# Performance work log

Measured on AMD Instinct MI355X. Metric: run time of the kernel, lower is better.

## Reference

```python
import jax, jax.numpy as jnp
import numpy as np

B, T, K, H = 8192, 96, 32, 768  # batch, max_len, output_dim (tags), bert hidden


def setup_inputs() -> dict:
    key = jax.random.key(0)
    k1, k2, k3, k4 = jax.random.split(key, 4)
    hidden = jax.random.normal(k1, (B, H), dtype=jnp.float32)
    target = jax.random.randint(k2, (B, T), 0, K, dtype=jnp.int32)
    # Dense(output_dim * max_len) params
    W = jax.random.normal(k3, (H, T * K), dtype=jnp.float32) * 0.02
    b = jnp.zeros((T * K,), dtype=jnp.float32)
    # tf.random.uniform transition matrix
    transitions = jax.random.uniform(k4, (K, K), dtype=jnp.float32)
    return {"hidden": hidden, "target": target, "W": W, "b": b, "transitions": transitions}


def _crf_log_norm(em_tm, transitions):
    # em_tm: [T, B, K] time-major emissions. Forward algorithm (logsumexp recurrence).
    def step(alpha, em_t):
        # alpha: [B, K]; broadcast over next-tag axis
        new = jax.nn.logsumexp(alpha[:, :, None] + transitions[None, :, :], axis=1) + em_t
        return new, None
    alpha, _ = jax.lax.scan(step, em_tm[0], em_tm[1:])
    return jax.nn.logsumexp(alpha, axis=-1)  # [B]


def _crf_sequence_score(em_btk, target, transitions):
    # unary: emission score at gold tags; binary: transition scores along gold path
    unary = jnp.take_along_axis(em_btk, target[..., None], axis=-1)[..., 0].sum(-1)
    binary = transitions[target[:, :-1], target[:, 1:]].sum(-1)
    return unary + binary  # [B]


def _viterbi_decode(em_tm, transitions):
    # em_tm: [T, B, K]. Max-product forward pass collecting backpointers.
    def fwd(v, em_t):
        scores = v[:, :, None] + transitions[None, :, :]  # [B, K_prev, K_next]
        bp = jnp.argmax(scores, axis=1).astype(jnp.int32)  # [B, K]
        return jnp.max(scores, axis=1) + em_t, bp
    v, bps = jax.lax.scan(fwd, em_tm[0], em_tm[1:])  # bps: [T-1, B, K]
    last_tag = jnp.argmax(v, axis=-1).astype(jnp.int32)  # [B]
    # backtrace (reverse scan); output index i is the tag at time i
    def back(tag, bp_t):
        prev = jnp.take_along_axis(bp_t, tag[:, None], axis=1)[:, 0]
        return prev, prev
    _, prevs = jax.lax.scan(back, last_tag, bps, reverse=True)  # [T-1, B]
    tags = jnp.concatenate([prevs, last_tag[None, :]], axis=0)  # [T, B]
    return jnp.transpose(tags), jnp.max(v, axis=-1)


def reference(hidden, target, W, b, transitions):
    # Dense with sigmoid, then reshape to (B, max_len, output_dim)
    em = jax.nn.sigmoid(hidden @ W + b).reshape(hidden.shape[0], T, K)
    em_tm = jnp.transpose(em, (1, 0, 2))  # time-major for scan
    log_likelihood = _crf_sequence_score(em, target, transitions) - _crf_log_norm(em_tm, transitions)
    decode_predict, _ = _viterbi_decode(em_tm, transitions)
    return decode_predict, log_likelihood
```

## Files before the change

### kernel.cpp

```cpp
#include <hip/hip_runtime.h>
#include <cstdint>
#include <cstddef>

#define B_  8192
#define T_  96
#define K_  32
#define H_  768
#define NK_ (T_ * K_)

typedef __attribute__((ext_vector_type(8))) _Float16 f16x8;
typedef __attribute__((ext_vector_type(4))) float    f32x4;

#define SCALE_UP   4096.0f
#define SCALE_DOWN (1.0f / 16777216.0f)

__device__ __forceinline__ void load_lds16(const void* g, void* l) {
    __builtin_amdgcn_global_load_lds(
        (const __attribute__((address_space(1))) unsigned int*)g,
        (__attribute__((address_space(3))) unsigned int*)l,
        16, 0, 0);
}

__global__ __launch_bounds__(256) void splitA_kernel(
    const float* __restrict__ A, _Float16* __restrict__ Ath, _Float16* __restrict__ Atl)
{
    const int g   = blockIdx.x * 256 + threadIdx.x;
    const int row = g / 96;
    const int o   = g - row * 96;
    const int ks  = o >> 2, qq = o & 3;
    const int r   = row & 127, rb = row >> 7;
    const size_t dst = (size_t)(rb * 24 + ks) * 4096 + r * 32 + ((qq ^ ((r >> 1) & 3)) << 3);

    f32x4 v0 = *(const f32x4*)(A + (size_t)row * H_ + o * 8);
    f32x4 v1 = *(const f32x4*)(A + (size_t)row * H_ + o * 8 + 4);
    f16x8 hi, lo;
#pragma unroll
    for (int e = 0; e < 8; e++) {
        float x = ((e < 4) ? v0[e] : v1[e - 4]) * SCALE_UP;
        _Float16 h = (_Float16)x;
        hi[e] = h;
        lo[e] = (_Float16)(x - (float)h);
    }
    *(f16x8*)&Ath[dst] = hi;
    *(f16x8*)&Atl[dst] = lo;
}

__global__ __launch_bounds__(256) void splitW_kernel(
    const float* __restrict__ W, _Float16* __restrict__ Wth, _Float16* __restrict__ Wtl)
{
    const int g   = blockIdx.x * 256 + threadIdx.x;
    const int ko  = g / NK_;
    const int col = g - ko * NK_;
    const int k0  = ko * 8;
    const int cb  = col >> 7, n = col & 127;
    const int ks  = k0 >> 5, qq = (k0 & 31) >> 3;
    const size_t dst = (size_t)(cb * 24 + ks) * 4096 + n * 32 + ((qq ^ ((n >> 1) & 3)) << 3);

    f16x8 hi, lo;
#pragma unroll
    for (int j = 0; j < 8; j++) {
        float x = W[(size_t)(k0 + j) * NK_ + col] * SCALE_UP;
        _Float16 h = (_Float16)x;
        hi[j] = h;
        lo[j] = (_Float16)(x - (float)h);
    }
    *(f16x8*)&Wth[dst] = hi;
    *(f16x8*)&Wtl[dst] = lo;
}

__global__ __launch_bounds__(256, 2) void gemm_mfma_sigmoid_kernel(
    const _Float16* __restrict__ Ath, const _Float16* __restrict__ Atl,
    const _Float16* __restrict__ Wth, const _Float16* __restrict__ Wtl,
    const float* __restrict__ bias, float* __restrict__ em)
{
    __shared__ _Float16 lds[2][4][4096];

    const int tid  = threadIdx.x;
    const int cb   = blockIdx.x;
    const int rb   = blockIdx.y;
    const int lane = tid & 63;
    const int w    = tid >> 6;
    const int wr   = w >> 1, wc = w & 1;
    const int fr   = lane & 15;
    const int kg   = lane >> 4;

    const _Float16* srcs[4] = {
        Ath + (size_t)(rb * 24) * 4096, Atl + (size_t)(rb * 24) * 4096,
        Wth + (size_t)(cb * 24) * 4096, Wtl + (size_t)(cb * 24) * 4096 };

    auto stage = [&](int ks, int bb) {
#pragma unroll
        for (int m = 0; m < 4; m++) {
            const _Float16* s = srcs[m] + (size_t)ks * 4096 + w * 1024 + lane * 8;
            _Float16* d = &lds[bb][m][w * 1024];
            load_lds16(s, d);
            load_lds16(s + 512, d + 512);
        }
    };

    f32x4 acc[4][4];
#pragma unroll
    for (int i = 0; i < 4; i++)
#pragma unroll
        for (int j = 0; j < 4; j++) acc[i][j] = (f32x4)0.0f;

    int cur = 0;
    stage(0, 0);

    for (int ks = 0; ks < 24; ks++) {
        __syncthreads();
        if (ks + 1 < 24) stage(ks + 1, cur ^ 1);

        f16x8 fah[4], fal[4], fbh[4], fbl[4];
#pragma unroll
        for (int mi = 0; mi < 4; mi++) {
            const int r   = wr * 64 + mi * 16 + fr;
            const int idx = r * 32 + ((kg ^ ((r >> 1) & 3)) << 3);
            fah[mi] = *(const f16x8*)&lds[cur][0][idx];
            fal[mi] = *(const f16x8*)&lds[cur][1][idx];
        }
#pragma unroll
        for (int ni = 0; ni < 4; ni++) {
            const int r   = wc * 64 + ni * 16 + fr;
            const int idx = r * 32 + ((kg ^ ((r >> 1) & 3)) << 3);
            fbh[ni] = *(const f16x8*)&lds[cur][2][idx];
            fbl[ni] = *(const f16x8*)&lds[cur][3][idx];
        }
#pragma unroll
        for (int mi = 0; mi < 4; mi++)
#pragma unroll
            for (int ni = 0; ni < 4; ni++) {
                acc[mi][ni] = __builtin_amdgcn_mfma_f32_16x16x32_f16(fah[mi], fbh[ni], acc[mi][ni], 0, 0, 0);
                acc[mi][ni] = __builtin_amdgcn_mfma_f32_16x16x32_f16(fah[mi], fbl[ni], acc[mi][ni], 0, 0, 0);
                acc[mi][ni] = __builtin_amdgcn_mfma_f32_16x16x32_f16(fal[mi], fbh[ni], acc[mi][ni], 0, 0, 0);
            }
        cur ^= 1;
    }

    const int er = rb * 128 + wr * 64 + (lane >> 4) * 4;
    const int ec = cb * 128 + wc * 64 + fr;
#pragma unroll
    for (int ni = 0; ni < 4; ni++) {
        const int   gc = ec + ni * 16;
        const float bv = bias[gc];
#pragma unroll
        for (int mi = 0; mi < 4; mi++)
#pragma unroll
            for (int r = 0; r < 4; r++) {
                const int gr = er + mi * 16 + r;
                float x = acc[mi][ni][r] * SCALE_DOWN + bv;
                em[(size_t)gr * NK_ + gc] = 1.0f / (1.0f + __expf(-x));
            }
    }
}

__global__ __launch_bounds__(256) void crf_scan_kernel(
    const float* __restrict__ em,
    const int* __restrict__ target,
    const float* __restrict__ trans,
    float* __restrict__ out_tags,
    float* __restrict__ ll)
{
    __shared__ float  trans_s[K_ * K_];
    __shared__ float4 ev4[8][16];
    __shared__ unsigned int bp_s[8][24][K_];

    const int tid = threadIdx.x;
    const int g   = tid >> 5;
    const int k   = tid & 31;
    const int b   = blockIdx.x * 8 + g;

    for (int i = tid; i < K_ * K_; i += 256) trans_s[i] = trans[i];
    __syncthreads();

    float tcol[K_], Ecol[K_];
#pragma unroll
    for (int p = 0; p < K_; p++) {
        tcol[p] = trans_s[p * K_ + k];
        Ecol[p] = __expf(tcol[p]);
    }

    const float* emb = em + (size_t)b * NK_;

    const float em0 = emb[k];
    float alpha = em0;
    float v     = em0;
    int   tgt_prev = target[b * T_];
    float unary  = (k == tgt_prev) ? em0 : 0.0f;
    float binary = 0.0f;
    unsigned int bpw = 0;

    float2* evp = (float2*)&ev4[g][0];

    for (int t = 1; t < T_; t++) {
        const float em_t = emb[t * K_ + k];

        float mh = alpha;
#pragma unroll
        for (int d = 16; d >= 1; d >>= 1) mh = fmaxf(mh, __shfl_xor(mh, d));
        const float e = __expf(alpha - mh);

        evp[k] = make_float2(e, v);
        __builtin_amdgcn_wave_barrier();

        float sum = 0.0f;
        float bv  = -1e30f;
        int   bi  = 0;
#pragma unroll
        for (int c = 0; c < 16; c++) {
            f32x4 q = *(const f32x4*)&ev4[g][c];
            const int p0 = 2 * c, p1 = 2 * c + 1;
            sum = fmaf(q[0], Ecol[p0], sum);
            float sv0 = q[1] + tcol[p0];
            if (sv0 > bv) { bv = sv0; bi = p0; }
            sum = fmaf(q[2], Ecol[p1], sum);
            float sv1 = q[3] + tcol[p1];
            if (sv1 > bv) { bv = sv1; bi = p1; }
        }

        alpha = mh + __logf(sum) + em_t;
        v     = bv + em_t;

        bpw |= (unsigned int)bi << (8 * ((t - 1) & 3));
        if (((t - 1) & 3) == 3) { bp_s[g][(t - 1) >> 2][k] = bpw; bpw = 0; }

        const int tgt = target[b * T_ + t];
        unary  += (k == tgt) ? em_t : 0.0f;
        binary += trans_s[tgt_prev * K_ + tgt];
        tgt_prev = tgt;
    }
    bp_s[g][23][k] = bpw;
    __builtin_amdgcn_wave_barrier();

    float m2 = alpha;
#pragma unroll
    for (int d = 16; d >= 1; d >>= 1) m2 = fmaxf(m2, __shfl_xor(m2, d));
    float s2 = __expf(alpha - m2);
#pragma unroll
    for (int d = 16; d >= 1; d >>= 1) s2 += __shfl_xor(s2, d);
    const float logZ = m2 + __logf(s2);

    float un = unary;
#pragma unroll
    for (int d = 16; d >= 1; d >>= 1) un += __shfl_xor(un, d);

    float bvv = v;
    int   bii = k;
#pragma unroll
    for (int d = 16; d >= 1; d >>= 1) {
        float ov = __shfl_xor(bvv, d);
        int   oi = __shfl_xor(bii, d);
        if (ov > bvv || (ov == bvv && oi < bii)) { bvv = ov; bii = oi; }
    }

    if (k == 0) {
        ll[b] = un + binary - logZ;
        float* ot = out_tags + (size_t)b * T_;
        int tag = bii;
        ot[T_ - 1] = (float)tag;
        for (int t = T_ - 2; t >= 0; t--) {
            unsigned int wd = bp_s[g][t >> 2][tag];
            tag = (wd >> (8 * (t & 3))) & 0xFF;
            ot[t] = (float)tag;
        }
    }
}

extern "C" void kernel_launch(void* const* d_in, const int* in_sizes, int n_in,
                              void* d_out, int out_size, void* d_ws, size_t ws_size,
                              hipStream_t stream)
{
    const float* hidden = (const float*)d_in[0];
    const int*   target = (const int*)d_in[1];
    const float* W      = (const float*)d_in[2];
    const float* bias   = (const float*)d_in[3];
    const float* trans  = (const float*)d_in[4];

    float* out      = (float*)d_out;
    float* out_tags = out;
    float* out_ll   = out + (size_t)B_ * T_;

    char* ws = (char*)d_ws;
    const size_t emB = (size_t)B_ * NK_ * 4;
    const size_t ahB = (size_t)B_ * H_ * 2;
    const size_t whB = (size_t)H_ * NK_ * 2;
    float*    em  = (float*)ws;
    _Float16* Ath = (_Float16*)(ws + emB);
    _Float16* Atl = (_Float16*)(ws + emB + ahB);
    _Float16* Wth = (_Float16*)(ws + emB + 2 * ahB);
    _Float16* Wtl = (_Float16*)(ws + emB + 2 * ahB + whB);

    splitA_kernel<<<(B_ * 96) / 256, 256, 0, stream>>>(hidden, Ath, Atl);
    splitW_kernel<<<(NK_ * 96) / 256, 256, 0, stream>>>(W, Wth, Wtl);

    dim3 gemm_grid(NK_ / 128, B_ / 128);
    gemm_mfma_sigmoid_kernel<<<gemm_grid, 256, 0, stream>>>(Ath, Atl, Wth, Wtl, bias, em);

    crf_scan_kernel<<<B_ / 8, 256, 0, stream>>>(em, target, trans, out_tags, out_ll);
}
```

Baseline: 300.8 us.

## Split CRF scan into forward and Viterbi waves, remap GEMM tiles per XCD

The CRF kernel now gives the forward (log-normalizer) recurrence and the Viterbi recurrence to separate wavefronts, so each sequence's two chains run in parallel rather than serially in one thread group. The forward pass moves to the linear exp domain with periodic power-of-two renormalization, which removes the per-step max, exp and log. The gold-path score is computed in parallel across time, and backpointers are packed at 5 bits each. The GEMM grid is flattened with a block-index swizzle that spreads neighbouring tiles across XCDs. This adds numerical risk from the exp-domain recurrence with its fixed offset of 4 per step.

New measurement: 250.5 us. -16.7%, faster.

```diff
diff --git a/kernel.cpp b/kernel.cpp
--- a/kernel.cpp
+++ b/kernel.cpp
@@ -76,8 +76,10 @@
     __shared__ _Float16 lds[2][4][4096];
 
     const int tid  = threadIdx.x;
-    const int cb   = blockIdx.x;
-    const int rb   = blockIdx.y;
+    const int bid  = blockIdx.x;
+    const int wgid = (bid & 7) * 192 + (bid >> 3);
+    const int cb   = wgid % 24;
+    const int rb   = wgid / 24;
     const int lane = tid & 63;
     const int w    = tid >> 6;
     const int wr   = w >> 1, wc = w & 1;
@@ -154,114 +156,165 @@
     }
 }
 
-__global__ __launch_bounds__(256) void crf_scan_kernel(
+
+#define VSTEP(T_, SH_, WI_)                                               \
+  {                                                                       \
+    const float cem = na; na = emb[((T_) + 1) * K_];                      \
+    vxs[k] = va;                                                          \
+    __builtin_amdgcn_wave_barrier();                                      \
+    float bva = -1e30f; int bia = 0;                                      \
+    _Pragma("unroll")                                                     \
+    for (int j = 0; j < 8; j++) {                                         \
+      f32x4 vq = *(const f32x4*)&vxs[4 * j];                              \
+      float s0 = vq[0] + tca[4 * j];                                      \
+      float s1 = vq[1] + tca[4 * j + 1];                                  \
+      float s2 = vq[2] + tca[4 * j + 2];                                  \
+      float s3 = vq[3] + tca[4 * j + 3];                                  \
+      float w0 = (s1 > s0) ? s1 : s0;                                     \
+      int   i0 = (s1 > s0) ? (4 * j + 1) : (4 * j);                       \
+      float w1 = (s3 > s2) ? s3 : s2;                                     \
+      int   i1 = (s3 > s2) ? (4 * j + 3) : (4 * j + 2);                   \
+      if (w1 > w0) { w0 = w1; i0 = i1; }                                  \
+      if (w0 > bva) { bva = w0; bia = i0; }                               \
+    }                                                                     \
+    va = bva + cem;                                                       \
+    bpw |= (unsigned int)bia << (5 * (SH_));                              \
+    if ((SH_) == 5) { bps[k * 17 + (WI_)] = bpw; bpw = 0; }               \
+    __builtin_amdgcn_wave_barrier();                                      \
+  }
+
+__global__ __launch_bounds__(256, 4) void crf_roles_kernel(
     const float* __restrict__ em,
     const int* __restrict__ target,
     const float* __restrict__ trans,
     float* __restrict__ out_tags,
     float* __restrict__ ll)
 {
-    __shared__ float  trans_s[K_ * K_];
-    __shared__ float4 ev4[8][16];
-    __shared__ unsigned int bp_s[8][24][K_];
-
-    const int tid = threadIdx.x;
-    const int g   = tid >> 5;
-    const int k   = tid & 31;
-    const int b   = blockIdx.x * 8 + g;
+    __shared__ float trans_s[K_ * K_];
+    __shared__ float Eex[4][36];
+    __shared__ float vex[4][36];
+    __shared__ unsigned int bp5[4][545];
+    __shared__ unsigned char tgt_s[4][T_];
+
+    const int tid  = threadIdx.x;
+    const int w    = tid >> 6;
+    const int lane = tid & 63;
+    const int half = lane >> 5;
+    const int k    = lane & 31;
+    const bool isFwd = (w < 2);
+    const int s    = (((isFwd ? w : w - 2) << 1) | half);
+    const int b    = blockIdx.x * 4 + s;
 
     for (int i = tid; i < K_ * K_; i += 256) trans_s[i] = trans[i];
     __syncthreads();
 
-    float tcol[K_], Ecol[K_];
-#pragma unroll
-    for (int p = 0; p < K_; p++) {
-        tcol[p] = trans_s[p * K_ + k];
-        Ecol[p] = __expf(tcol[p]);
-    }
-
-    const float* emb = em + (size_t)b * NK_;
-
-    const float em0 = emb[k];
-    float alpha = em0;
-    float v     = em0;
-    int   tgt_prev = target[b * T_];
-    float unary  = (k == tgt_prev) ? em0 : 0.0f;
-    float binary = 0.0f;
-    unsigned int bpw = 0;
-
-    float2* evp = (float2*)&ev4[g][0];
-
-    for (int t = 1; t < T_; t++) {
-        const float em_t = emb[t * K_ + k];
-
-        float mh = alpha;
-#pragma unroll
-        for (int d = 16; d >= 1; d >>= 1) mh = fmaxf(mh, __shfl_xor(mh, d));
-        const float e = __expf(alpha - mh);
-
-        evp[k] = make_float2(e, v);
+    const float* emb = em + (size_t)b * NK_ + k;
+
+    if (isFwd) {
+        float Ea2[K_];
+#pragma unroll
+        for (int p = 0; p < K_; p++) Ea2[p] = __expf(trans_s[p * K_ + k]);
+
+        const int t0 = target[b * T_ + k];
+        const int t1 = target[b * T_ + 32 + k];
+        const int t2 = target[b * T_ + 64 + k];
+        tgt_s[s][k]      = (unsigned char)t0;
+        tgt_s[s][k + 32] = (unsigned char)t1;
+        tgt_s[s][k + 64] = (unsigned char)t2;
         __builtin_amdgcn_wave_barrier();
-
-        float sum = 0.0f;
-        float bv  = -1e30f;
-        int   bi  = 0;
-#pragma unroll
-        for (int c = 0; c < 16; c++) {
-            f32x4 q = *(const f32x4*)&ev4[g][c];
-            const int p0 = 2 * c, p1 = 2 * c + 1;
-            sum = fmaf(q[0], Ecol[p0], sum);
-            float sv0 = q[1] + tcol[p0];
-            if (sv0 > bv) { bv = sv0; bi = p0; }
-            sum = fmaf(q[2], Ecol[p1], sum);
-            float sv1 = q[3] + tcol[p1];
-            if (sv1 > bv) { bv = sv1; bi = p1; }
-        }
-
-        alpha = mh + __logf(sum) + em_t;
-        v     = bv + em_t;
-
-        bpw |= (unsigned int)bi << (8 * ((t - 1) & 3));
-        if (((t - 1) & 3) == 3) { bp_s[g][(t - 1) >> 2][k] = bpw; bpw = 0; }
-
-        const int tgt = target[b * T_ + t];
-        unary  += (k == tgt) ? em_t : 0.0f;
-        binary += trans_s[tgt_prev * K_ + tgt];
-        tgt_prev = tgt;
-    }
-    bp_s[g][23][k] = bpw;
-    __builtin_amdgcn_wave_barrier();
-
-    float m2 = alpha;
-#pragma unroll
-    for (int d = 16; d >= 1; d >>= 1) m2 = fmaxf(m2, __shfl_xor(m2, d));
-    float s2 = __expf(alpha - m2);
-#pragma unroll
-    for (int d = 16; d >= 1; d >>= 1) s2 += __shfl_xor(s2, d);
-    const float logZ = m2 + __logf(s2);
-
-    float un = unary;
-#pragma unroll
-    for (int d = 16; d >= 1; d >>= 1) un += __shfl_xor(un, d);
-
-    float bvv = v;
-    int   bii = k;
-#pragma unroll
-    for (int d = 16; d >= 1; d >>= 1) {
-        float ov = __shfl_xor(bvv, d);
-        int   oi = __shfl_xor(bii, d);
-        if (ov > bvv || (ov == bvv && oi < bii)) { bvv = ov; bii = oi; }
-    }
-
-    if (k == 0) {
-        ll[b] = un + binary - logZ;
-        float* ot = out_tags + (size_t)b * T_;
-        int tag = bii;
-        ot[T_ - 1] = (float)tag;
-        for (int t = T_ - 2; t >= 0; t--) {
-            unsigned int wd = bp_s[g][t >> 2][tag];
-            tag = (wd >> (8 * (t & 3))) & 0xFF;
-            ot[t] = (float)tag;
+        const float* emrow = em + (size_t)b * NK_;
+        float gold = emrow[k * K_ + t0] + emrow[(k + 32) * K_ + t1] + emrow[(k + 64) * K_ + t2];
+        if (k > 0) gold += trans_s[(int)tgt_s[s][k - 1] * K_ + t0];
+        gold += trans_s[(int)tgt_s[s][k + 31] * K_ + t1];
+        gold += trans_s[(int)tgt_s[s][k + 63] * K_ + t2];
+
+        float Ea = __expf(emb[0]);
+        int   expo_sum = 0;
+        float na = emb[K_];
+        float* exs = &Eex[s][0];
+
+        for (int t = 1; t <= 95; ++t) {
+            const float cem = na;
+            na = emb[(t + 1) * K_];
+            exs[k] = Ea;
+            __builtin_amdgcn_wave_barrier();
+            float fa = 0.0f;
+#pragma unroll
+            for (int j = 0; j < 8; j++) {
+                f32x4 q = *(const f32x4*)&exs[4 * j];
+                fa = fmaf(q[0], Ea2[4 * j],     fa);
+                fa = fmaf(q[1], Ea2[4 * j + 1], fa);
+                fa = fmaf(q[2], Ea2[4 * j + 2], fa);
+                fa = fmaf(q[3], Ea2[4 * j + 3], fa);
+            }
+            Ea = fa * __expf(cem - 4.0f);
+            __builtin_amdgcn_wave_barrier();
+
+            if ((t % 12) == 0) {
+                float m = Ea;
+#pragma unroll
+                for (int d = 16; d >= 1; d >>= 1) m = fmaxf(m, __shfl_xor(m, d));
+                const unsigned int ebits = (__float_as_uint(m) >> 23) & 255u;
+                const float sc = __uint_as_float((254u - ebits) << 23);
+                Ea *= sc;
+                expo_sum += (int)ebits - 127;
+            }
+        }
+
+        float S = Ea;
+#pragma unroll
+        for (int d = 16; d >= 1; d >>= 1) S += __shfl_xor(S, d);
+        const float logZ = __logf(S) + 380.0f + (float)expo_sum * 0.69314718055994531f;
+
+        float gs = gold;
+#pragma unroll
+        for (int d = 16; d >= 1; d >>= 1) gs += __shfl_xor(gs, d);
+
+        if (k == 0) ll[b] = gs - logZ;
+
+    } else {
+        float tca[K_];
+#pragma unroll
+        for (int p = 0; p < K_; p++) tca[p] = trans_s[p * K_ + k];
+
+        float va = emb[0];
+        float na = emb[K_];
+        unsigned int bpw = 0;
+        float* vxs = &vex[s][0];
+        unsigned int* bps = &bp5[s][0];
+
+        for (int it = 0; it < 7; ++it) {
+            const int tb = it * 12 + 1;
+            const int wi = it * 2;
+            VSTEP(tb + 0, 0, wi)  VSTEP(tb + 1, 1, wi)  VSTEP(tb + 2, 2, wi)
+            VSTEP(tb + 3, 3, wi)  VSTEP(tb + 4, 4, wi)  VSTEP(tb + 5, 5, wi)
+            VSTEP(tb + 6, 0, wi + 1)  VSTEP(tb + 7, 1, wi + 1)  VSTEP(tb + 8, 2, wi + 1)
+            VSTEP(tb + 9, 3, wi + 1)  VSTEP(tb + 10, 4, wi + 1) VSTEP(tb + 11, 5, wi + 1)
+        }
+        VSTEP(85, 0, 14) VSTEP(86, 1, 14) VSTEP(87, 2, 14)
+        VSTEP(88, 3, 14) VSTEP(89, 4, 14) VSTEP(90, 5, 14)
+        VSTEP(91, 0, 15) VSTEP(92, 1, 15) VSTEP(93, 2, 15)
+        VSTEP(94, 3, 15) VSTEP(95, 4, 15)
+        bps[k * 17 + 15] = bpw;
+        __builtin_amdgcn_wave_barrier();
+
+        float bv = va; int bi = k;
+#pragma unroll
+        for (int d = 16; d >= 1; d >>= 1) {
+            float ov = __shfl_xor(bv, d);
+            int   oi = __shfl_xor(bi, d);
+            if (ov > bv || (ov == bv && oi < bi)) { bv = ov; bi = oi; }
+        }
+
+        if (k == 0) {
+            float* ot = out_tags + (size_t)b * T_;
+            int tag = bi;
+            ot[T_ - 1] = (float)tag;
+            for (int t = T_ - 2; t >= 0; t--) {
+                unsigned int wd = bps[tag * 17 + t / 6];
+                tag = (int)((wd >> (5 * (t % 6))) & 31u);
+                ot[t] = (float)tag;
+            }
         }
     }
 }
@@ -284,6 +337,7 @@
     const size_t emB = (size_t)B_ * NK_ * 4;
     const size_t ahB = (size_t)B_ * H_ * 2;
     const size_t whB = (size_t)H_ * NK_ * 2;
+
     float*    em  = (float*)ws;
     _Float16* Ath = (_Float16*)(ws + emB);
     _Float16* Atl = (_Float16*)(ws + emB + ahB);
@@ -293,8 +347,7 @@
     splitA_kernel<<<(B_ * 96) / 256, 256, 0, stream>>>(hidden, Ath, Atl);
     splitW_kernel<<<(NK_ * 96) / 256, 256, 0, stream>>>(W, Wth, Wtl);
 
-    dim3 gemm_grid(NK_ / 128, B_ / 128);
-    gemm_mfma_sigmoid_kernel<<<gemm_grid, 256, 0, stream>>>(Ath, Atl, Wth, Wtl, bias, em);
-
-    crf_scan_kernel<<<B_ / 8, 256, 0, stream>>>(em, target, trans, out_tags, out_ll);
-}
+    gemm_mfma_sigmoid_kernel<<<1536, 256, 0, stream>>>(Ath, Atl, Wth, Wtl, bias, em);
+
+    crf_roles_kernel<<<B_ / 4, 256, 0, stream>>>(em, target, trans, out_tags, out_ll);
+}
```
